# Kernel optimization log

Hardware: AMD Instinct MI355X
Metric: run time of the kernel (lower is better)

Reference implementation:

```python
import jax, jax.numpy as jnp
import numpy as np

N = 8192        # batch_size == num nodes == num hyperedges
D = 512         # hidden_dim
H_HEADS = 8
HD = D // H_HEADS
TOP_K = 16
EPS = 1e-5      # LayerNorm eps


def setup_inputs() -> dict:
    key = jax.random.key(0)
    ks = jax.random.split(key, 10)
    def rn(k, shape, scale=0.02):
        return jax.random.normal(k, shape, dtype=jnp.float32) * scale
    return {
        "x0": jax.random.normal(ks[0], (N, D), dtype=jnp.float32),
        "x1": jax.random.normal(ks[1], (N, D), dtype=jnp.float32),
        # modality projections: Linear -> ReLU -> LayerNorm (per modality)
        "w_p0": rn(ks[2], (D, D)), "b_p0": jnp.zeros((D,), jnp.float32),
        "g0": jnp.ones((D,), jnp.float32), "beta0": jnp.zeros((D,), jnp.float32),
        "w_p1": rn(ks[3], (D, D)), "b_p1": jnp.zeros((D,), jnp.float32),
        "g1": jnp.ones((D,), jnp.float32), "beta1": jnp.zeros((D,), jnp.float32),
        # MultiheadAttention packed in-proj + out-proj
        "in_w": rn(ks[4], (3 * D, D)), "in_b": jnp.zeros((3 * D,), jnp.float32),
        "out_w": rn(ks[5], (D, D)), "out_b": jnp.zeros((D,), jnp.float32),
        # edge weight predictor MLP
        "ew_w1": rn(ks[6], (D // 2, D)), "ew_b1": jnp.zeros((D // 2,), jnp.float32),
        "ew_w2": rn(ks[7], (1, D // 2)), "ew_b2": jnp.zeros((1,), jnp.float32),
    }


def _layernorm(x, g, b):
    m = x.mean(-1, keepdims=True)
    v = ((x - m) ** 2).mean(-1, keepdims=True)
    return (x - m) * jax.lax.rsqrt(v + EPS) * g + b


def _forward(x0, x1, w_p0, b_p0, g0, beta0, w_p1, b_p1, g1, beta1,
             in_w, in_b, out_w, out_b, ew_w1, ew_b1, ew_w2, ew_b2):
    # per-modality projection: Linear -> ReLU -> LayerNorm
    p0 = _layernorm(jax.nn.relu(x0 @ w_p0.T + b_p0), g0, beta0)
    p1 = _layernorm(jax.nn.relu(x1 @ w_p1.T + b_p1), g1, beta1)
    seq = jnp.stack([p0, p1], axis=1)                       # [N, 2, D]
    # cross-modal MHA (self-attention over the 2 modality tokens)
    qkv = seq @ in_w.T + in_b                               # [N, 2, 3D]
    q, k, v = jnp.split(qkv, 3, axis=-1)
    q = q.reshape(N, 2, H_HEADS, HD)
    k = k.reshape(N, 2, H_HEADS, HD)
    v = v.reshape(N, 2, H_HEADS, HD)
    scores = jnp.einsum('bqhd,bkhd->bhqk', q, k) / jnp.sqrt(jnp.float32(HD))
    attn = jax.nn.softmax(scores, axis=-1)                  # [N, h, 2, 2]
    ctx = jnp.einsum('bhqk,bkhd->bqhd', attn, v).reshape(N, 2, D)
    attended = ctx @ out_w.T + out_b                        # [N, 2, D]
    fused = attended.mean(axis=1)                           # [N, D]
    # node-node attention similarity, row-softmax
    sim = jax.nn.softmax(fused @ fused.T, axis=1)           # [N, N]
    _, idx = jax.lax.top_k(sim, TOP_K)                      # [N, K]
    vals = jnp.take_along_axis(sim, idx, axis=1)            # [N, K]
    rows = jnp.arange(N)
    # H[i,i]=1 first, then H[neighbor, i] = sim[i, neighbor] (may overwrite diag)
    H = jnp.zeros((N, N), sim.dtype).at[rows, rows].set(1.0)
    H = H.at[idx, rows[:, None]].set(vals)
    colsum = H.sum(axis=0)
    H = H.at[rows, rows].set(jnp.where(colsum == 0, 1.0, H[rows, rows]))
    # edge weights
    hidden = jax.nn.relu(fused @ ew_w1.T + ew_b1)
    ew = jax.nn.sigmoid(hidden @ ew_w2.T + ew_b2)[:, 0]     # [N]
    ew = jnp.maximum(ew, 1e-8)
    return H, ew


def reference(x0, x1, w_p0, b_p0, g0, beta0, w_p1, b_p1, g1, beta1,
              in_w, in_b, out_w, out_b, ew_w1, ew_b1, ew_w2, ew_b2):
    return _forward(x0, x1, w_p0, b_p0, g0, beta0, w_p1, b_p1, g1, beta1,
                    in_w, in_b, out_w, out_b, ew_w1, ew_b1, ew_w2, ew_b2)
```

## Files before the change

kernel.cpp:

```cpp
#include <hip/hip_runtime.h>
#include <hip/hip_bf16.h>

#define NN 8192
#define DD 512

typedef unsigned short u16;
typedef __bf16 bf16_t;
typedef bf16_t bf16x8 __attribute__((ext_vector_type(8)));
typedef float f32x4 __attribute__((ext_vector_type(4)));

__device__ __forceinline__ float bf2f(u16 h) {
    union { unsigned u; float f; } v; v.u = ((unsigned)h) << 16; return v.f;
}
__device__ __forceinline__ float bflo(unsigned u) {
    union { unsigned u; float f; } v; v.u = u << 16; return v.f;
}
__device__ __forceinline__ float bfhi(unsigned u) {
    union { unsigned u; float f; } v; v.u = u & 0xFFFF0000u; return v.f;
}
__device__ __forceinline__ u16 f2bf(float f) {
    union { float f; unsigned u; } v; v.f = f;
    unsigned r = v.u + 0x7fffu + ((v.u >> 16) & 1u);
    return (u16)(r >> 16);
}

__global__ __launch_bounds__(256) void cvt7(
        const float* __restrict__ s0, u16* __restrict__ d0,
        const float* __restrict__ s1, u16* __restrict__ d1,
        const float* __restrict__ s2, u16* __restrict__ d2,
        const float* __restrict__ s3, u16* __restrict__ d3,
        const float* __restrict__ s4, u16* __restrict__ d4,
        const float* __restrict__ s5, u16* __restrict__ d5,
        const float* __restrict__ s6, u16* __restrict__ d6) {
    size_t v = ((size_t)blockIdx.x * 256 + threadIdx.x) * 8;
    const float* s; u16* d; size_t off;
    if (v < 4194304)      { s = s0; d = d0; off = v; }
    else if (v < 8388608) { s = s1; d = d1; off = v - 4194304; }
    else if (v < 8650752) { s = s2; d = d2; off = v - 8388608; }
    else if (v < 8912896) { s = s3; d = d3; off = v - 8650752; }
    else if (v < 9699328) { s = s4; d = d4; off = v - 8912896; }
    else if (v < 9961472) { s = s5; d = d5; off = v - 9699328; }
    else                  { s = s6; d = d6; off = v - 9961472; }
    float4 a = *(const float4*)(s + off);
    float4 b = *(const float4*)(s + off + 4);
    ushort4 o0 = make_ushort4(f2bf(a.x), f2bf(a.y), f2bf(a.z), f2bf(a.w));
    ushort4 o1 = make_ushort4(f2bf(b.x), f2bf(b.y), f2bf(b.z), f2bf(b.w));
    *(ushort4*)(d + off) = o0;
    *(ushort4*)(d + off + 4) = o1;
}

#define EPS_LDS 136
template<bool RELU, bool BIAS, bool SPLIT>
__global__ __launch_bounds__(256) void gemm_bt(const u16* __restrict__ A,
        const u16* __restrict__ B, const float* __restrict__ bias,
        const u16* __restrict__ B2, const float* __restrict__ bias2, int halfY,
        u16* __restrict__ C, int M, int Nc, int K) {
    __shared__ alignas(16) u16 Smem[128 * EPS_LDS];
    u16* As = Smem;
    u16* Bs = Smem + 128 * 64;
    const int t = threadIdx.x;
    const int lane = t & 63;
    const int wave = t >> 6;
    const int wm = (wave >> 1) * 64;
    const int wn = (wave & 1) * 64;
    const int rowA = blockIdx.y * 128;
    const int rowB = blockIdx.x * 128;
    if (SPLIT && (int)blockIdx.y >= halfY) { B = B2; bias = bias2; }

    f32x4 acc[4][4] = {};

    const int mrow = lane & 15;
    const int kk = (lane >> 4) * 8;

    for (int k0 = 0; k0 < K; k0 += 64) {
        __syncthreads();
        #pragma unroll
        for (int r = 0; r < 4; ++r) {
            int chunk = r * 256 + t;
            const u16* srcA = A + (size_t)(rowA + (chunk >> 3)) * K + k0 + (chunk & 7) * 8;
            __builtin_amdgcn_global_load_lds(
                (const __attribute__((address_space(1))) void*)srcA,
                (__attribute__((address_space(3))) void*)(As + chunk * 8), 16, 0, 0);
            const u16* srcB = B + (size_t)(rowB + (chunk >> 3)) * K + k0 + (chunk & 7) * 8;
            __builtin_amdgcn_global_load_lds(
                (const __attribute__((address_space(1))) void*)srcB,
                (__attribute__((address_space(3))) void*)(Bs + chunk * 8), 16, 0, 0);
        }
        __syncthreads();
        #pragma unroll
        for (int ks = 0; ks < 64; ks += 32) {
            bf16x8 af[4], bfv[4];
            #pragma unroll
            for (int i = 0; i < 4; ++i)
                af[i] = *(const bf16x8*)(As + (wm + i * 16 + mrow) * 64 + ks + kk);
            #pragma unroll
            for (int j = 0; j < 4; ++j)
                bfv[j] = *(const bf16x8*)(Bs + (wn + j * 16 + mrow) * 64 + ks + kk);
            #pragma unroll
            for (int i = 0; i < 4; ++i)
                #pragma unroll
                for (int j = 0; j < 4; ++j)
                    acc[i][j] = __builtin_amdgcn_mfma_f32_16x16x32_bf16(af[i], bfv[j], acc[i][j], 0, 0, 0);
        }
    }

    __syncthreads();
    const int er0 = wm + (lane >> 4) * 4;
    const int ec0 = wn + (lane & 15);
    #pragma unroll
    for (int j = 0; j < 4; ++j) {
        int c = ec0 + j * 16;
        float bv = BIAS ? bias[rowB + c] : 0.0f;
        #pragma unroll
        for (int i = 0; i < 4; ++i) {
            #pragma unroll
            for (int r = 0; r < 4; ++r) {
                float v = acc[i][j][r] + bv;
                if (RELU) v = fmaxf(v, 0.0f);
                Smem[(er0 + i * 16 + r) * EPS_LDS + c] = f2bf(v);
            }
        }
    }
    __syncthreads();
    #pragma unroll
    for (int pass = 0; pass < 8; ++pass) {
        int chunk = pass * 256 + t;
        int rloc = chunk >> 4, coff = (chunk & 15) * 8;
        bf16x8 v = *(const bf16x8*)(Smem + rloc * EPS_LDS + coff);
        *(bf16x8*)(C + (size_t)(rowA + rloc) * Nc + rowB + coff) = v;
    }
}

__global__ __launch_bounds__(256) void ln2_kernel(const u16* __restrict__ y,
        const float* __restrict__ g0, const float* __restrict__ b0,
        const float* __restrict__ g1, const float* __restrict__ b1,
        u16* __restrict__ seq) {
    __shared__ float sred[4];
    int n = blockIdx.x, t = threadIdx.x;
    int modality = n >> 13, node = n & (NN - 1);
    const float* g = modality ? g1 : g0;
    const float* b = modality ? b1 : b0;
    const u16* yr = y + (size_t)n * DD;
    float x0 = bf2f(yr[t]), x1 = bf2f(yr[t + 256]);
    float s = x0 + x1;
    for (int off = 32; off; off >>= 1) s += __shfl_xor(s, off);
    if ((t & 63) == 0) sred[t >> 6] = s;
    __syncthreads();
    float mean = (sred[0] + sred[1] + sred[2] + sred[3]) * (1.0f / DD);
    __syncthreads();
    float d0 = x0 - mean, d1 = x1 - mean;
    float vs = d0 * d0 + d1 * d1;
    for (int off = 32; off; off >>= 1) vs += __shfl_xor(vs, off);
    if ((t & 63) == 0) sred[t >> 6] = vs;
    __syncthreads();
    float var = (sred[0] + sred[1] + sred[2] + sred[3]) * (1.0f / DD);
    float inv = rsqrtf(var + 1e-5f);
    u16* out = seq + (size_t)node * (2 * DD) + modality * DD;
    out[t]       = f2bf(d0 * inv * g[t]       + b[t]);
    out[t + 256] = f2bf(d1 * inv * g[t + 256] + b[t + 256]);
}

__global__ __launch_bounds__(256) void attn_kernel(const u16* __restrict__ qkv,
        u16* __restrict__ ctxm) {
    int gid = blockIdx.x * 4 + (threadIdx.x >> 6);
    int lane = threadIdx.x & 63;
    int n = gid >> 3, h = gid & 7;
    const u16* r0 = qkv + (size_t)(n * 2) * 1536;
    const u16* r1 = r0 + 1536;
    float q0 = bf2f(r0[h * 64 + lane]);
    float k0 = bf2f(r0[512 + h * 64 + lane]);
    float v0 = bf2f(r0[1024 + h * 64 + lane]);
    float q1 = bf2f(r1[h * 64 + lane]);
    float k1 = bf2f(r1[512 + h * 64 + lane]);
    float v1 = bf2f(r1[1024 + h * 64 + lane]);
    float p00 = q0 * k0, p01 = q0 * k1, p10 = q1 * k0, p11 = q1 * k1;
    for (int off = 32; off; off >>= 1) {
        p00 += __shfl_xor(p00, off);
        p01 += __shfl_xor(p01, off);
        p10 += __shfl_xor(p10, off);
        p11 += __shfl_xor(p11, off);
    }
    const float sc = 0.125f;
    float s00 = p00 * sc, s01 = p01 * sc, s10 = p10 * sc, s11 = p11 * sc;
    float m0 = fmaxf(s00, s01), e00 = __expf(s00 - m0), e01 = __expf(s01 - m0);
    float a00 = e00 / (e00 + e01), a01 = e01 / (e00 + e01);
    float m1 = fmaxf(s10, s11), e10 = __expf(s10 - m1), e11 = __expf(s11 - m1);
    float a10 = e10 / (e10 + e11), a11 = e11 / (e10 + e11);
    float c0 = a00 * v0 + a01 * v1;
    float c1 = a10 * v0 + a11 * v1;
    ctxm[(size_t)n * 512 + h * 64 + lane] = f2bf(0.5f * (c0 + c1));
}

__global__ __launch_bounds__(256) void topk_bf16(const u16* __restrict__ S,
        float* __restrict__ topv, int* __restrict__ topi) {
    const float NEG = -3e38f;
    int row = blockIdx.x * 4 + (threadIdx.x >> 6);
    int lane = threadIdx.x & 63;
    const u16* Sr = S + (size_t)row * NN;

    float m = NEG, l = 0.0f;
    float t1v = NEG, t2v = NEG;
    int t1i = 0x7FFFFFFF, t2i = 0x7FFFFFFF;

    #pragma unroll
    for (int p = 0; p < 16; ++p) {
        uint4 raw = *(const uint4*)(Sr + p * 512 + lane * 8);
        int base = p * 512 + lane * 8;
        #pragma unroll
        for (int q = 0; q < 4; ++q) {
            unsigned w = (&raw.x)[q];
            #pragma unroll
            for (int h = 0; h < 2; ++h) {
                float x = h ? bfhi(w) : bflo(w);
                int xi = base + q * 2 + h;
                if (x > m) { l = l * __expf(m - x) + 1.0f; m = x; }
                else l += __expf(x - m);
                bool g1 = x > t1v, g2 = x > t2v;
                t2v = g1 ? t1v : (g2 ? x : t2v);
                t2i = g1 ? t1i : (g2 ? xi : t2i);
                t1v = g1 ? x : t1v;
                t1i = g1 ? xi : t1i;
            }
        }
    }
    #pragma unroll
    for (int off = 32; off; off >>= 1) {
        float om = __shfl_xor(m, off);
        float ol = __shfl_xor(l, off);
        float nm = fmaxf(m, om);
        l = l * __expf(m - nm) + ol * __expf(om - nm);
        m = nm;
    }

    unsigned mk0 = 0, mk1 = 0, mk2 = 0, mk3 = 0;
    float cv = t1v; int ci = t1i;
    float bv = t2v; int bi = t2i;
    for (int r = 0; r < 16; ++r) {
        float wv = cv; int wi = ci;
        #pragma unroll
        for (int off = 32; off; off >>= 1) {
            float ov = __shfl_xor(wv, off);
            int oi = __shfl_xor(wi, off);
            if (ov > wv || (ov == wv && oi < wi)) { wv = ov; wi = oi; }
        }
        if (lane == 0) {
            topv[(size_t)row * 16 + r] = __expf(wv - m) / l;
            topi[(size_t)row * 16 + r] = wi;
        }
        if (wi == ci) {
            int slot = ((wi >> 9) << 3) | (wi & 7);
            unsigned bit = 1u << (slot & 31);
            if (slot < 32) mk0 |= bit; else if (slot < 64) mk1 |= bit;
            else if (slot < 96) mk2 |= bit; else mk3 |= bit;
            cv = bv; ci = bi;
            bv = NEG; bi = 0x7FFFFFFF;
            if (ci == 0x7FFFFFFF) {
                float nb = NEG; int ni = 0x7FFFFFFF;
                #pragma unroll
                for (int p = 0; p < 16; ++p) {
                    uint4 raw = *(const uint4*)(Sr + p * 512 + lane * 8);
                    int base = p * 512 + lane * 8;
                    #pragma unroll
                    for (int q = 0; q < 4; ++q) {
                        unsigned w = (&raw.x)[q];
                        #pragma unroll
                        for (int h = 0; h < 2; ++h) {
                            int sl = p * 8 + q * 2 + h;
                            unsigned mw = (sl < 32) ? mk0 : (sl < 64) ? mk1
                                        : (sl < 96) ? mk2 : mk3;
                            float x = ((mw >> (sl & 31)) & 1u) ? NEG
                                    : (h ? bfhi(w) : bflo(w));
                            if (x > nb) { nb = x; ni = base + q * 2 + h; }
                        }
                    }
                }
                cv = nb; ci = ni;
            }
        }
    }
}

__global__ __launch_bounds__(256) void scatter_diag(const float* __restrict__ topv,
        const int* __restrict__ topi, float* __restrict__ H) {
    int tk = blockIdx.x * 256 + threadIdx.x;
    if (tk < NN * 16) {
        int i = tk >> 4;
        int idx = topi[tk];
        H[(size_t)idx * NN + i] = topv[tk];
    } else {
        int c = tk - NN * 16;
        const int* ti = topi + c * 16;
        bool self = false;
        #pragma unroll
        for (int j = 0; j < 16; ++j) self |= (ti[j] == c);
        if (!self) H[(size_t)c * NN + c] = 1.0f;
    }
}

__global__ __launch_bounds__(256) void ew_kernel(const u16* __restrict__ hidden,
        const float* __restrict__ w2, const float* __restrict__ b2, float* __restrict__ out) {
    int n = blockIdx.x * 4 + (threadIdx.x >> 6);
    int lane = threadIdx.x & 63;
    const u16* hr = hidden + (size_t)n * 256;
    float s = 0.0f;
    #pragma unroll
    for (int p = 0; p < 4; ++p) s += bf2f(hr[lane + p * 64]) * w2[lane + p * 64];
    for (int off = 32; off; off >>= 1) s += __shfl_xor(s, off);
    if (lane == 0) {
        float z = s + b2[0];
        float sig = 1.0f / (1.0f + __expf(-z));
        out[n] = fmaxf(sig, 1e-8f);
    }
}

extern "C" void kernel_launch(void* const* d_in, const int* in_sizes, int n_in,
                              void* d_out, int out_size, void* d_ws, size_t ws_size,
                              hipStream_t stream) {
    const float* x0    = (const float*)d_in[0];
    const float* x1    = (const float*)d_in[1];
    const float* w_p0  = (const float*)d_in[2];
    const float* b_p0  = (const float*)d_in[3];
    const float* g0    = (const float*)d_in[4];
    const float* beta0 = (const float*)d_in[5];
    const float* w_p1  = (const float*)d_in[6];
    const float* b_p1  = (const float*)d_in[7];
    const float* g1    = (const float*)d_in[8];
    const float* beta1 = (const float*)d_in[9];
    const float* in_w  = (const float*)d_in[10];
    const float* in_b  = (const float*)d_in[11];
    const float* out_w = (const float*)d_in[12];
    const float* out_b = (const float*)d_in[13];
    const float* ew_w1 = (const float*)d_in[14];
    const float* ew_b1 = (const float*)d_in[15];
    const float* ew_w2 = (const float*)d_in[16];
    const float* ew_b2 = (const float*)d_in[17];

    float* Hf = (float*)d_out;
    float* ew_out = Hf + (size_t)NN * NN;

    u16* Hu = (u16*)d_out;
    u16* x0b    = Hu;
    u16* x1b    = Hu + 4194304;
    u16* y01    = Hu + 8388608;
    u16* seq    = Hu + 16777216;
    u16* qkv    = Hu + 25165824;
    u16* ctxm   = Hu + 50331648;
    u16* hidden = Hu + 54525952;
    u16* wp0b   = Hu + 60817408;
    u16* wp1b   = wp0b + 262144;
    u16* inwb   = wp1b + 262144;
    u16* outwb  = inwb + 786432;
    u16* eww1b  = outwb + 262144;
    u16* Sb     = Hu + 67108864;
    char* ws = (char*)d_ws;
    u16* fusedB = (u16*)ws;
    float* topv = (float*)(ws + (8u << 20));
    int*   topi = (int*)(ws + (8u << 20) + 524288);

    dim3 blk(256);
    const int BIG = 1 << 30;
    cvt7<<<dim3(4928), blk, 0, stream>>>(x0, x0b, x1, x1b, w_p0, wp0b, w_p1, wp1b,
                                         in_w, inwb, out_w, outwb, ew_w1, eww1b);
    gemm_bt<true, true, true><<<dim3(4, 128), blk, 0, stream>>>(
        x0b, wp0b, b_p0, wp1b, b_p1, 64, y01, 2 * NN, DD, DD);
    ln2_kernel<<<dim3(2 * NN), blk, 0, stream>>>(y01, g0, beta0, g1, beta1, seq);
    gemm_bt<false, true, false><<<dim3(12, 128), blk, 0, stream>>>(
        seq, inwb, in_b, nullptr, nullptr, BIG, qkv, 2 * NN, 1536, DD);
    attn_kernel<<<dim3(NN * 8 / 4), blk, 0, stream>>>(qkv, ctxm);
    gemm_bt<false, true, false><<<dim3(4, 64), blk, 0, stream>>>(
        ctxm, outwb, out_b, nullptr, nullptr, BIG, fusedB, NN, DD, DD);
    gemm_bt<true, true, false><<<dim3(2, 64), blk, 0, stream>>>(
        fusedB, eww1b, ew_b1, nullptr, nullptr, BIG, hidden, NN, 256, DD);
    ew_kernel<<<dim3(NN / 4), blk, 0, stream>>>(hidden, ew_w2, ew_b2, ew_out);
    gemm_bt<false, false, false><<<dim3(64, 64), blk, 0, stream>>>(
        fusedB, fusedB, nullptr, nullptr, nullptr, BIG, Sb, NN, NN, DD);
    topk_bf16<<<dim3(NN / 4), blk, 0, stream>>>(Sb, topv, topi);
    hipMemsetAsync(Hf, 0, (size_t)NN * NN * sizeof(float), stream);
    scatter_diag<<<dim3((NN * 16 + NN) / 256), blk, 0, stream>>>(topv, topi, Hf);
}
```

Baseline: 711.9 us.

## Exploit symmetry of fused·fusedᵀ to compute only upper-triangle tiles

Replaces the general N×N similarity GEMM with a symmetric kernel that computes only tiles with bx>=by and writes each off-diagonal tile twice, once directly and once transposed through LDS. This roughly halves the MFMA work and the operand loads for the 8192×8192 product. In exchange, half the launched blocks exit immediately, and the transposed write reads LDS element by element with an odd stride (129), which may be slow. The bf16 output write traffic stays the same.

```diff
diff --git a/kernel.cpp b/kernel.cpp
--- a/kernel.cpp
+++ b/kernel.cpp
@@ -68,7 +68,6 @@
     if (SPLIT && (int)blockIdx.y >= halfY) { B = B2; bias = bias2; }
 
     f32x4 acc[4][4] = {};
-
     const int mrow = lane & 15;
     const int kk = (lane >> 4) * 8;
 
@@ -128,6 +127,94 @@
         int rloc = chunk >> 4, coff = (chunk & 15) * 8;
         bf16x8 v = *(const bf16x8*)(Smem + rloc * EPS_LDS + coff);
         *(bf16x8*)(C + (size_t)(rowA + rloc) * Nc + rowB + coff) = v;
+    }
+}
+
+#define SYM_LDS 129
+__global__ __launch_bounds__(256) void gemm_sym(const u16* __restrict__ F,
+        u16* __restrict__ C) {
+    __shared__ alignas(16) u16 Smem[128 * SYM_LDS];
+    const int bx = blockIdx.x, by = blockIdx.y;
+    if (bx < by) return;
+    u16* As = Smem;
+    u16* Bs = Smem + 128 * 64;
+    const int t = threadIdx.x;
+    const int lane = t & 63;
+    const int wave = t >> 6;
+    const int wm = (wave >> 1) * 64;
+    const int wn = (wave & 1) * 64;
+    const int rowI = by * 128;
+    const int rowJ = bx * 128;
+
+    f32x4 acc[4][4] = {};
+    const int mrow = lane & 15;
+    const int kk = (lane >> 4) * 8;
+
+    for (int k0 = 0; k0 < DD; k0 += 64) {
+        __syncthreads();
+        #pragma unroll
+        for (int r = 0; r < 4; ++r) {
+            int chunk = r * 256 + t;
+            const u16* srcA = F + (size_t)(rowI + (chunk >> 3)) * DD + k0 + (chunk & 7) * 8;
+            __builtin_amdgcn_global_load_lds(
+                (const __attribute__((address_space(1))) void*)srcA,
+                (__attribute__((address_space(3))) void*)(As + chunk * 8), 16, 0, 0);
+            const u16* srcB = F + (size_t)(rowJ + (chunk >> 3)) * DD + k0 + (chunk & 7) * 8;
+            __builtin_amdgcn_global_load_lds(
+                (const __attribute__((address_space(1))) void*)srcB,
+                (__attribute__((address_space(3))) void*)(Bs + chunk * 8), 16, 0, 0);
+        }
+        __syncthreads();
+        #pragma unroll
+        for (int ks = 0; ks < 64; ks += 32) {
+            bf16x8 af[4], bfv[4];
+            #pragma unroll
+            for (int i = 0; i < 4; ++i)
+                af[i] = *(const bf16x8*)(As + (wm + i * 16 + mrow) * 64 + ks + kk);
+            #pragma unroll
+            for (int j = 0; j < 4; ++j)
+                bfv[j] = *(const bf16x8*)(Bs + (wn + j * 16 + mrow) * 64 + ks + kk);
+            #pragma unroll
+            for (int i = 0; i < 4; ++i)
+                #pragma unroll
+                for (int j = 0; j < 4; ++j)
+                    acc[i][j] = __builtin_amdgcn_mfma_f32_16x16x32_bf16(af[i], bfv[j], acc[i][j], 0, 0, 0);
+        }
+    }
+
+    __syncthreads();
+    const int er0 = wm + (lane >> 4) * 4;
+    const int ec0 = wn + (lane & 15);
+    #pragma unroll
+    for (int j = 0; j < 4; ++j) {
+        int c = ec0 + j * 16;
+        #pragma unroll
+        for (int i = 0; i < 4; ++i) {
+            #pragma unroll
+            for (int r = 0; r < 4; ++r)
+                Smem[(er0 + i * 16 + r) * SYM_LDS + c] = f2bf(acc[i][j][r]);
+        }
+    }
+    __syncthreads();
+    #pragma unroll
+    for (int pass = 0; pass < 8; ++pass) {
+        int chunk = pass * 256 + t;
+        int rloc = chunk >> 4, coff = (chunk & 15) * 8;
+        union { u16 us[8]; bf16x8 v; } buf;
+        #pragma unroll
+        for (int k = 0; k < 8; ++k) buf.us[k] = Smem[rloc * SYM_LDS + coff + k];
+        *(bf16x8*)(C + (size_t)(rowI + rloc) * NN + rowJ + coff) = buf.v;
+    }
+    if (bx != by) {
+        #pragma unroll
+        for (int pass = 0; pass < 8; ++pass) {
+            int chunk = pass * 256 + t;
+            int tr = chunk >> 4, roff = (chunk & 15) * 8;
+            union { u16 us[8]; bf16x8 v; } buf;
+            #pragma unroll
+            for (int k = 0; k < 8; ++k) buf.us[k] = Smem[(roff + k) * SYM_LDS + tr];
+            *(bf16x8*)(C + (size_t)(rowJ + tr) * NN + rowI + roff) = buf.v;
+        }
     }
 }
 
@@ -372,8 +459,7 @@
     gemm_bt<true, true, false><<<dim3(2, 64), blk, 0, stream>>>(
         fusedB, eww1b, ew_b1, nullptr, nullptr, BIG, hidden, NN, 256, DD);
     ew_kernel<<<dim3(NN / 4), blk, 0, stream>>>(hidden, ew_w2, ew_b2, ew_out);
-    gemm_bt<false, false, false><<<dim3(64, 64), blk, 0, stream>>>(
-        fusedB, fusedB, nullptr, nullptr, nullptr, BIG, Sb, NN, NN, DD);
+    gemm_sym<<<dim3(64, 64), blk, 0, stream>>>(fusedB, Sb);
     topk_bf16<<<dim3(NN / 4), blk, 0, stream>>>(Sb, topv, topi);
     hipMemsetAsync(Hf, 0, (size_t)NN * NN * sizeof(float), stream);
     scatter_diag<<<dim3((NN * 16 + NN) / 256), blk, 0, stream>>>(topv, topi, Hf);
```

After: 690.9 us. -3.0%, faster.
